# Optimization experiments

Measured on AMD Instinct MI355X. Metric: run time of the kernel, lower is better.

## Reference

```python
import jax, jax.numpy as jnp
import numpy as np

N = 50_000          # nodes (spots)
E = 800_000         # edges (~kNN degree 16)
IN_DIM, HID, OUT = 512, 64, 32
LEAKY = 0.2


def setup_inputs() -> dict:
    key = jax.random.key(0)
    ks = jax.random.split(key, 8)
    features = jax.random.normal(ks[0], (N, IN_DIM), dtype=jnp.float32)
    edge_index = jax.random.randint(ks[1], (2, E), 0, N, dtype=jnp.int64)
    # tied-weight GAT autoencoder parameters (xavier-normal, gain=1.414 as in stGCL)
    W1 = (jax.random.normal(ks[2], (IN_DIM, HID), dtype=jnp.float32)
          * np.float32(1.414 / np.sqrt(IN_DIM)))
    a1_src = jax.random.normal(ks[3], (HID,), dtype=jnp.float32) * 0.1
    a1_dst = jax.random.normal(ks[4], (HID,), dtype=jnp.float32) * 0.1
    W2 = (jax.random.normal(ks[5], (HID, OUT), dtype=jnp.float32)
          * np.float32(1.414 / np.sqrt(HID)))
    a3_src = jax.random.normal(ks[6], (HID,), dtype=jnp.float32) * 0.1
    a3_dst = jax.random.normal(ks[7], (HID,), dtype=jnp.float32) * 0.1
    return {"features": features, "edge_index": edge_index,
            "W1": W1, "a1_src": a1_src, "a1_dst": a1_dst,
            "W2": W2, "a3_src": a3_src, "a3_dst": a3_dst}


def reference(features, edge_index, W1, a1_src, a1_dst, W2, a3_src, a3_dst):
    src, dst = edge_index[0], edge_index[1]
    n = features.shape[0]

    # torch.randperm(features.size(0)) -> fixed-seed permutation
    perm = jax.random.permutation(jax.random.key(42), n)
    rand_features = features[perm]

    def gat(x, W, a_s, a_d):
        # stGCL GATConv (heads=1, concat=False, no self loops, no bias):
        # x_src = x_dst = x @ W; edge score = leaky_relu(a_s.xw[src] + a_d.xw[dst])
        xw = x @ W                                             # [N, C]
        e = jax.nn.leaky_relu((xw @ a_s)[src] + (xw @ a_d)[dst],
                              negative_slope=LEAKY)            # [E]
        # per-destination segment softmax (PyG softmax semantics)
        m = jax.ops.segment_max(e, dst, num_segments=n)        # [N]
        ex = jnp.exp(e - m[dst])
        denom = jax.ops.segment_sum(ex, dst, num_segments=n)
        alpha = ex / (denom[dst] + 1e-16)                      # [E]
        # weighted scatter-add aggregation
        return jax.ops.segment_sum(xw[src] * alpha[:, None], dst,
                                   num_segments=n)             # [N, C]

    def encode_decode(x):
        h1 = jax.nn.elu(gat(x, W1, a1_src, a1_dst))            # conv1, attention
        h2 = h1 @ W2                                           # conv2, attention=False
        h3 = jax.nn.elu(gat(h2, W2.T, a3_src, a3_dst))         # conv3 (tied W2^T), attention
        h4 = h3 @ W1.T                                         # conv4 (tied W1^T), attention=False
        return h2, h4

    h2, h4 = encode_decode(features)
    rand_h2, rand_h4 = encode_decode(rand_features)
    summary = jax.nn.sigmoid(h2.mean(axis=0))                  # [OUT]
    return (h2, h4, h4, rand_h2, rand_h4, rand_h4, summary)
```

## Files before the change

### kernel.cpp

```cpp
#include <hip/hip_runtime.h>
#include <hip/hip_bf16.h>
#include <vector>
#include <algorithm>
#include <cstring>
#include <cstdint>

#define NN 50000
#define EE 800000

static inline uint32_t rotl32(uint32_t v, int r) { return (v << r) | (v >> (32 - r)); }

static inline void tf2x32(uint32_t k0, uint32_t k1, uint32_t& x0, uint32_t& x1) {
  uint32_t ks0 = k0, ks1 = k1, ks2 = k0 ^ k1 ^ 0x1BD11BDAu;
  const int r1[4] = {13, 15, 26, 6}, r2[4] = {17, 29, 16, 24};
  x0 += ks0; x1 += ks1;
  for (int i = 0; i < 4; i++) { x0 += x1; x1 = rotl32(x1, r1[i]); x1 ^= x0; }
  x0 += ks1; x1 += ks2 + 1u;
  for (int i = 0; i < 4; i++) { x0 += x1; x1 = rotl32(x1, r2[i]); x1 ^= x0; }
  x0 += ks2; x1 += ks0 + 2u;
  for (int i = 0; i < 4; i++) { x0 += x1; x1 = rotl32(x1, r1[i]); x1 ^= x0; }
  x0 += ks0; x1 += ks1 + 3u;
  for (int i = 0; i < 4; i++) { x0 += x1; x1 = rotl32(x1, r2[i]); x1 ^= x0; }
  x0 += ks1; x1 += ks2 + 4u;
  for (int i = 0; i < 4; i++) { x0 += x1; x1 = rotl32(x1, r1[i]); x1 ^= x0; }
  x0 += ks2; x1 += ks0 + 5u;
}

static void compute_perm(int* perm, int n) {
  std::vector<uint32_t> sk(n);
  std::vector<int> val(n), order(n), nv(n);
  for (int i = 0; i < n; i++) val[i] = i;
  uint32_t k0 = 0u, k1 = 42u;
  for (int round = 0; round < 2; ++round) {
    uint32_t nk0, nk1, sk0, sk1;
    { uint32_t a = 0, b = 0; tf2x32(k0, k1, a, b); nk0 = a; nk1 = b; }
    { uint32_t a = 0, b = 1; tf2x32(k0, k1, a, b); sk0 = a; sk1 = b; }
    for (int i = 0; i < n; i++) {
      uint32_t a = 0, b = (uint32_t)i;
      tf2x32(sk0, sk1, a, b);
      sk[i] = a ^ b;
    }
    for (int i = 0; i < n; i++) order[i] = i;
    std::stable_sort(order.begin(), order.end(),
                     [&](int x, int y) { return sk[x] < sk[y]; });
    for (int i = 0; i < n; i++) nv[i] = val[order[i]];
    val.swap(nv);
    k0 = nk0; k1 = nk1;
  }
  std::memcpy(perm, val.data(), (size_t)n * sizeof(int));
}

struct PermHolder {
  int perm[NN];
  PermHolder() { compute_perm(perm, NN); }
};
static const PermHolder g_perm;


__global__ void count_kernel(const int* __restrict__ ei, int* __restrict__ counts, int E) {
  int e = blockIdx.x * 256 + threadIdx.x;
  if (e < E) atomicAdd(&counts[ei[E + e]], 1);
}

__global__ __launch_bounds__(1024) void scan_kernel(const int* __restrict__ counts,
                                                    int* __restrict__ offsets, int n) {
  __shared__ int wsum[16];
  __shared__ int wscan[16];
  __shared__ int carry_s;
  int tid = threadIdx.x, lane = tid & 63, wid = tid >> 6;
  if (tid == 0) carry_s = 0;
  __syncthreads();
  for (int base = 0; base < n; base += 1024) {
    int i = base + tid;
    int v = (i < n) ? counts[i] : 0;
    int x = v;
    #pragma unroll
    for (int off = 1; off < 64; off <<= 1) {
      int t = __shfl_up(x, off);
      if (lane >= off) x += t;
    }
    if (lane == 63) wsum[wid] = x;
    __syncthreads();
    if (wid == 0) {
      int wv = (lane < 16) ? wsum[lane] : 0;
      #pragma unroll
      for (int off = 1; off < 16; off <<= 1) {
        int t = __shfl_up(wv, off);
        if (lane >= off) wv += t;
      }
      if (lane < 16) wscan[lane] = wv;
    }
    __syncthreads();
    int wbase = (wid == 0) ? 0 : wscan[wid - 1];
    int carry = carry_s;
    if (i < n) offsets[i] = carry + wbase + x - v;
    int total = wscan[15];
    __syncthreads();
    if (tid == 0) carry_s = carry + total;
    __syncthreads();
  }
  if (threadIdx.x == 0) offsets[n] = carry_s;
}

__global__ void scatter_kernel(const int* __restrict__ ei, const int* __restrict__ offsets,
                               int* __restrict__ cursor, int* __restrict__ srcs, int E) {
  int e = blockIdx.x * 256 + threadIdx.x;
  if (e >= E) return;
  int s = ei[e];
  int d = ei[E + e];
  int pos = offsets[d] + atomicAdd(&cursor[d], 1);
  srcs[pos] = s;
}

__global__ __launch_bounds__(256) void gemm1_kernel(const float* __restrict__ A,
                                                    const float* __restrict__ B,
                                                    float* __restrict__ C,
                                                    const int* __restrict__ gather, int n) {
  __shared__ float As[32][68];
  __shared__ float Bs[32][68];
  int t = threadIdx.x;
  int m0 = blockIdx.x * 64;
  int tr = t >> 4, tc = t & 15;
  float acc[4][4] = {};
  for (int k0 = 0; k0 < 512; k0 += 32) {
    #pragma unroll
    for (int q = 0; q < 2; ++q) {
      int f = t + q * 256;
      int r = f >> 3, kq = f & 7;
      int row = m0 + r; row = (row < n) ? row : (n - 1);
      int g = gather ? gather[row] : row;
      const float4 av = *(const float4*)(A + (size_t)g * 512 + k0 + kq * 4);
      As[kq * 4 + 0][r] = av.x; As[kq * 4 + 1][r] = av.y;
      As[kq * 4 + 2][r] = av.z; As[kq * 4 + 3][r] = av.w;
    }
    #pragma unroll
    for (int q = 0; q < 2; ++q) {
      int f = t + q * 256;
      int kk = f >> 4, cq = f & 15;
      const float4 bv = *(const float4*)(B + (size_t)(k0 + kk) * 64 + cq * 4);
      *(float4*)(&Bs[kk][cq * 4]) = bv;
    }
    __syncthreads();
    #pragma unroll
    for (int kk = 0; kk < 32; ++kk) {
      float a[4], b[4];
      #pragma unroll
      for (int i = 0; i < 4; i++) a[i] = As[kk][tr * 4 + i];
      #pragma unroll
      for (int j = 0; j < 4; j++) b[j] = Bs[kk][tc * 4 + j];
      #pragma unroll
      for (int i = 0; i < 4; i++)
        #pragma unroll
        for (int j = 0; j < 4; j++) acc[i][j] += a[i] * b[j];
    }
    __syncthreads();
  }
  #pragma unroll
  for (int i = 0; i < 4; i++) {
    int row = m0 + tr * 4 + i;
    if (row < n) {
      float4 v = {acc[i][0], acc[i][1], acc[i][2], acc[i][3]};
      *(float4*)(C + (size_t)row * 64 + tc * 4) = v;
    }
  }
}

__global__ void dots_kernel(const float* __restrict__ xw, const float* __restrict__ a_src,
                            const float* __restrict__ a_dst, float* __restrict__ s,
                            float* __restrict__ d, int n) {
  int w = (blockIdx.x * blockDim.x + threadIdx.x) >> 6;
  int lane = threadIdx.x & 63;
  if (w >= n) return;
  float v = xw[(size_t)w * 64 + lane];
  float vs = v * a_src[lane], vd = v * a_dst[lane];
  #pragma unroll
  for (int off = 32; off; off >>= 1) {
    vs += __shfl_down(vs, off);
    vd += __shfl_down(vd, off);
  }
  if (lane == 0) { s[w] = vs; d[w] = vd; }
}

__global__ __launch_bounds__(256) void gat_kernel(const int* __restrict__ offs,
                                                  const int* __restrict__ srcs,
                                                  const float* __restrict__ s,
                                                  const float* __restrict__ dvec,
                                                  const float* __restrict__ xw,
                                                  float* __restrict__ h, int n) {
  int w = (blockIdx.x * blockDim.x + threadIdx.x) >> 6;
  int lane = threadIdx.x & 63;
  if (w >= n) return;
  int start = offs[w], end = offs[w + 1];
  float dd = dvec[w];
  float m = -INFINITY;
  for (int j = start + lane; j < end; j += 64) {
    float e = s[srcs[j]] + dd;
    e = e > 0.f ? e : 0.2f * e;
    m = fmaxf(m, e);
  }
  #pragma unroll
  for (int off = 32; off; off >>= 1) m = fmaxf(m, __shfl_xor(m, off));
  float sum = 0.f;
  for (int j = start + lane; j < end; j += 64) {
    float e = s[srcs[j]] + dd;
    e = e > 0.f ? e : 0.2f * e;
    sum += __expf(e - m);
  }
  #pragma unroll
  for (int off = 32; off; off >>= 1) sum += __shfl_xor(sum, off);
  float inv = 1.0f / (sum + 1e-16f);
  float acc = 0.f;
  for (int j = start; j < end; ++j) {
    int sj = srcs[j];
    float e = s[sj] + dd;
    e = e > 0.f ? e : 0.2f * e;
    float alpha = __expf(e - m) * inv;
    acc += alpha * xw[(size_t)sj * 64 + lane];
  }
  h[(size_t)w * 64 + lane] = acc > 0.f ? acc : expm1f(acc);
}

__global__ void gemm2_kernel(const float* __restrict__ h1, const float* __restrict__ W2,
                             float* __restrict__ h2, int n) {
  int id = blockIdx.x * 256 + threadIdx.x;
  if (id >= n * 32) return;
  int i = id >> 5, c = id & 31;
  float sacc = 0.f;
  #pragma unroll
  for (int k = 0; k < 64; k++) sacc += h1[(size_t)i * 64 + k] * W2[k * 32 + c];
  h2[id] = sacc;
}

__global__ void gemm3_kernel(const float* __restrict__ h2, const float* __restrict__ W2,
                             float* __restrict__ xw3, int n) {
  int id = blockIdx.x * 256 + threadIdx.x;
  if (id >= n * 64) return;
  int i = id >> 6, c = id & 63;
  float sacc = 0.f;
  #pragma unroll
  for (int j = 0; j < 32; j++) sacc += h2[(size_t)i * 32 + j] * W2[c * 32 + j];
  xw3[id] = sacc;
}

__global__ __launch_bounds__(256) void gemm4_kernel(const float* __restrict__ A,
                                                    const float* __restrict__ W1,
                                                    float* __restrict__ C0,
                                                    float* __restrict__ C1, int n) {
  __shared__ float As[64][68];
  __shared__ float Bs[64][68];
  int t = threadIdx.x;
  int m0 = blockIdx.x * 64;
  int o0 = blockIdx.y * 64;
  int tr = t >> 4, tc = t & 15;
  #pragma unroll
  for (int q = 0; q < 4; ++q) {
    int f = t + q * 256;
    int r = f >> 4, cq = f & 15;
    int row = m0 + r; row = (row < n) ? row : (n - 1);
    const float4 av = *(const float4*)(A + (size_t)row * 64 + cq * 4);
    As[cq * 4 + 0][r] = av.x; As[cq * 4 + 1][r] = av.y;
    As[cq * 4 + 2][r] = av.z; As[cq * 4 + 3][r] = av.w;
  }
  #pragma unroll
  for (int q = 0; q < 4; ++q) {
    int f = t + q * 256;
    int o = f >> 4, cq = f & 15;
    const float4 wv = *(const float4*)(W1 + (size_t)(o0 + o) * 64 + cq * 4);
    Bs[cq * 4 + 0][o] = wv.x; Bs[cq * 4 + 1][o] = wv.y;
    Bs[cq * 4 + 2][o] = wv.z; Bs[cq * 4 + 3][o] = wv.w;
  }
  __syncthreads();
  float acc[4][4] = {};
  #pragma unroll
  for (int kk = 0; kk < 64; ++kk) {
    float a[4], b[4];
    #pragma unroll
    for (int i = 0; i < 4; i++) a[i] = As[kk][tr * 4 + i];
    #pragma unroll
    for (int j = 0; j < 4; j++) b[j] = Bs[kk][tc * 4 + j];
    #pragma unroll
    for (int i = 0; i < 4; i++)
      #pragma unroll
      for (int j = 0; j < 4; j++) acc[i][j] += a[i] * b[j];
  }
  #pragma unroll
  for (int i = 0; i < 4; i++) {
    int row = m0 + tr * 4 + i;
    if (row < n) {
      float4 v = {acc[i][0], acc[i][1], acc[i][2], acc[i][3]};
      *(float4*)(C0 + (size_t)row * 512 + o0 + tc * 4) = v;
      *(float4*)(C1 + (size_t)row * 512 + o0 + tc * 4) = v;
    }
  }
}

__global__ void colsum_kernel(const float* __restrict__ h2, float* __restrict__ acc, int n) {
  int c = threadIdx.x & 31;
  int rg = (blockIdx.x << 3) + (threadIdx.x >> 5);
  float sloc = 0.f;
  for (int r = rg; r < n; r += 2048) sloc += h2[(size_t)r * 32 + c];
  atomicAdd(&acc[c], sloc);
}

__global__ void finalize_kernel(const float* __restrict__ acc, float* __restrict__ outp, int n) {
  int c = threadIdx.x;
  if (c < 32) {
    float mval = acc[c] / (float)n;
    outp[c] = 1.0f / (1.0f + __expf(-mval));
  }
}

extern "C" void kernel_launch(void* const* d_in, const int* in_sizes, int n_in,
                              void* d_out, int out_size, void* d_ws, size_t ws_size,
                              hipStream_t stream) {
  const float* features = (const float*)d_in[0];
  const int*   ei       = (const int*)d_in[1];
  const float* W1       = (const float*)d_in[2];
  const float* a1s      = (const float*)d_in[3];
  const float* a1d      = (const float*)d_in[4];
  const float* W2       = (const float*)d_in[5];
  const float* a3s      = (const float*)d_in[6];
  const float* a3d      = (const float*)d_in[7];
  float* out = (float*)d_out;

  const size_t NOUT = (size_t)NN * 32;
  const size_t NH4  = (size_t)NN * 512;
  const size_t OFF1 = NOUT;
  const size_t OFF2 = OFF1 + NH4;
  const size_t OFF3 = OFF2 + NH4;
  const size_t OFF4 = OFF3 + NOUT;
  const size_t OFF5 = OFF4 + NH4;
  const size_t OFF6 = OFF5 + NH4;

  char* w = (char*)d_ws;
  size_t o = 0;
  auto alloc = [&](size_t bytes) -> void* {
    void* p = w + o;
    o = (o + bytes + 255) & ~(size_t)255;
    return p;
  };
  int*   d_perm  = (int*)alloc((size_t)NN * 4);
  int*   counts  = (int*)alloc((size_t)NN * 4);
  int*   offsets = (int*)alloc((size_t)(NN + 1) * 4);
  int*   cursor  = (int*)alloc((size_t)NN * 4);
  int*   srcs    = (int*)alloc((size_t)EE * 4);
  float* xw      = (float*)alloc((size_t)NN * 64 * 4);
  float* hbuf    = (float*)alloc((size_t)NN * 64 * 4);
  float* sbuf    = (float*)alloc((size_t)NN * 4);
  float* dbuf    = (float*)alloc((size_t)NN * 4);
  float* accbuf  = (float*)alloc(32 * 4);

  hipMemcpyAsync(d_perm, g_perm.perm, (size_t)NN * 4, hipMemcpyHostToDevice, stream);
  hipMemsetAsync(counts, 0, (size_t)NN * 4, stream);
  hipMemsetAsync(cursor, 0, (size_t)NN * 4, stream);
  hipMemsetAsync(accbuf, 0, 32 * 4, stream);

  count_kernel<<<(EE + 255) / 256, 256, 0, stream>>>(ei, counts, EE);
  scan_kernel<<<1, 1024, 0, stream>>>(counts, offsets, NN);
  scatter_kernel<<<(EE + 255) / 256, 256, 0, stream>>>(ei, offsets, cursor, srcs, EE);

  const int rowBlocks = (NN + 63) / 64;
  const int nodeWaveBlocks = (NN * 64 + 255) / 256;

  for (int b = 0; b < 2; ++b) {
    const int* g = b ? d_perm : nullptr;
    float* h2out = out + (b ? OFF3 : 0);
    float* h4a   = out + (b ? OFF4 : OFF1);
    float* h4b   = out + (b ? OFF5 : OFF2);

    gemm1_kernel<<<rowBlocks, 256, 0, stream>>>(features, W1, xw, g, NN);
    dots_kernel<<<nodeWaveBlocks, 256, 0, stream>>>(xw, a1s, a1d, sbuf, dbuf, NN);
    gat_kernel<<<nodeWaveBlocks, 256, 0, stream>>>(offsets, srcs, sbuf, dbuf, xw, hbuf, NN);
    gemm2_kernel<<<(NN * 32 + 255) / 256, 256, 0, stream>>>(hbuf, W2, h2out, NN);
    gemm3_kernel<<<(NN * 64 + 255) / 256, 256, 0, stream>>>(h2out, W2, xw, NN);
    dots_kernel<<<nodeWaveBlocks, 256, 0, stream>>>(xw, a3s, a3d, sbuf, dbuf, NN);
    gat_kernel<<<nodeWaveBlocks, 256, 0, stream>>>(offsets, srcs, sbuf, dbuf, xw, hbuf, NN);
    gemm4_kernel<<<dim3(rowBlocks, 8), 256, 0, stream>>>(hbuf, W1, h4a, h4b, NN);
  }

  colsum_kernel<<<256, 256, 0, stream>>>(out, accbuf, NN);
  finalize_kernel<<<1, 64, 0, stream>>>(accbuf, out + OFF6, NN);
}
```

Baseline: 1.602 ms.

## Replace global-atomic CSR build with chunked LDS histogram counting sort

Replaces the global atomic count and scatter that build the destination-sorted edge list with a two-pass chunked counting sort. Per-chunk histograms are kept in LDS as packed 16-bit pairs, reduced and prefix-summed into per-chunk base offsets, and then each chunk scatters sources using LDS atomics for their ranks. This aims to remove contention on global atomics and to make the edge order within each destination deterministic. In exchange it adds kernels and a large per-chunk base array (CHUNKS*NN words) that must be written and read, and the 16-bit packing limits per-chunk degree.

```diff
diff --git a/kernel.cpp b/kernel.cpp
--- a/kernel.cpp
+++ b/kernel.cpp
@@ -7,6 +7,12 @@
 
 #define NN 50000
 #define EE 800000
+
+#define CHUNKS 128
+#define CHUNK_E (EE / CHUNKS)
+#define PAIRS (NN / 2)
+#define HALF (NN / 2)
+#define HPAIRS (HALF / 2)
 
 static inline uint32_t rotl32(uint32_t v, int r) { return (v << r) | (v >> (32 - r)); }
 
@@ -57,9 +63,35 @@
 static const PermHolder g_perm;
 
 
-__global__ void count_kernel(const int* __restrict__ ei, int* __restrict__ counts, int E) {
-  int e = blockIdx.x * 256 + threadIdx.x;
-  if (e < E) atomicAdd(&counts[ei[E + e]], 1);
+__global__ __launch_bounds__(256) void hist_kernel(const int* __restrict__ ei,
+                                                   uint32_t* __restrict__ hist) {
+  __shared__ uint32_t cnt[HPAIRS];
+  int b = blockIdx.x, c = b >> 1, h = b & 1;
+  for (int i = threadIdx.x; i < HPAIRS; i += 256) cnt[i] = 0;
+  __syncthreads();
+  int e0 = c * CHUNK_E;
+  int dlo = h * HALF;
+  for (int t = threadIdx.x; t < CHUNK_E; t += 256) {
+    int d = ei[EE + e0 + t];
+    int dl = d - dlo;
+    if ((unsigned)dl < (unsigned)HALF)
+      atomicAdd(&cnt[dl >> 1], (dl & 1) ? 0x10000u : 1u);
+  }
+  __syncthreads();
+  uint32_t* outp = hist + (size_t)c * PAIRS + (size_t)h * HPAIRS;
+  for (int i = threadIdx.x; i < HPAIRS; i += 256) outp[i] = cnt[i];
+}
+
+__global__ void counts_kernel(const uint32_t* __restrict__ hist, int* __restrict__ counts) {
+  int dp = blockIdx.x * 256 + threadIdx.x;
+  if (dp >= PAIRS) return;
+  uint32_t lo = 0, hi = 0;
+  for (int c = 0; c < CHUNKS; ++c) {
+    uint32_t p = hist[(size_t)c * PAIRS + dp];
+    lo += p & 0xFFFFu; hi += p >> 16;
+  }
+  counts[2 * dp] = (int)lo;
+  counts[2 * dp + 1] = (int)hi;
 }
 
 __global__ __launch_bounds__(1024) void scan_kernel(const int* __restrict__ counts,
@@ -102,14 +134,40 @@
   if (threadIdx.x == 0) offsets[n] = carry_s;
 }
 
-__global__ void scatter_kernel(const int* __restrict__ ei, const int* __restrict__ offsets,
-                               int* __restrict__ cursor, int* __restrict__ srcs, int E) {
-  int e = blockIdx.x * 256 + threadIdx.x;
-  if (e >= E) return;
-  int s = ei[e];
-  int d = ei[E + e];
-  int pos = offsets[d] + atomicAdd(&cursor[d], 1);
-  srcs[pos] = s;
+__global__ void base_kernel(const uint32_t* __restrict__ hist, const int* __restrict__ offsets,
+                            uint32_t* __restrict__ basearr) {
+  int dp = blockIdx.x * 256 + threadIdx.x;
+  if (dp >= PAIRS) return;
+  uint32_t r0 = (uint32_t)offsets[2 * dp];
+  uint32_t r1 = (uint32_t)offsets[2 * dp + 1];
+  for (int c = 0; c < CHUNKS; ++c) {
+    uint32_t p = hist[(size_t)c * PAIRS + dp];
+    basearr[(size_t)c * NN + 2 * dp] = r0;
+    basearr[(size_t)c * NN + 2 * dp + 1] = r1;
+    r0 += p & 0xFFFFu; r1 += p >> 16;
+  }
+}
+
+__global__ __launch_bounds__(256) void scatter2_kernel(const int* __restrict__ ei,
+                                                       const uint32_t* __restrict__ basearr,
+                                                       int* __restrict__ srcs) {
+  __shared__ uint32_t cnt[HPAIRS];
+  int b = blockIdx.x, c = b >> 1, h = b & 1;
+  for (int i = threadIdx.x; i < HPAIRS; i += 256) cnt[i] = 0;
+  __syncthreads();
+  int e0 = c * CHUNK_E;
+  int dlo = h * HALF;
+  const uint32_t* baserow = basearr + (size_t)c * NN;
+  for (int t = threadIdx.x; t < CHUNK_E; t += 256) {
+    int s = ei[e0 + t];
+    int d = ei[EE + e0 + t];
+    int dl = d - dlo;
+    if ((unsigned)dl < (unsigned)HALF) {
+      uint32_t old = atomicAdd(&cnt[dl >> 1], (dl & 1) ? 0x10000u : 1u);
+      uint32_t rank = (dl & 1) ? (old >> 16) : (old & 0xFFFFu);
+      srcs[baserow[d] + rank] = s;
+    }
+  }
 }
 
 __global__ __launch_bounds__(256) void gemm1_kernel(const float* __restrict__ A,
@@ -339,25 +397,26 @@
     o = (o + bytes + 255) & ~(size_t)255;
     return p;
   };
-  int*   d_perm  = (int*)alloc((size_t)NN * 4);
-  int*   counts  = (int*)alloc((size_t)NN * 4);
-  int*   offsets = (int*)alloc((size_t)(NN + 1) * 4);
-  int*   cursor  = (int*)alloc((size_t)NN * 4);
-  int*   srcs    = (int*)alloc((size_t)EE * 4);
-  float* xw      = (float*)alloc((size_t)NN * 64 * 4);
-  float* hbuf    = (float*)alloc((size_t)NN * 64 * 4);
-  float* sbuf    = (float*)alloc((size_t)NN * 4);
-  float* dbuf    = (float*)alloc((size_t)NN * 4);
-  float* accbuf  = (float*)alloc(32 * 4);
+  int*      d_perm  = (int*)alloc((size_t)NN * 4);
+  int*      counts  = (int*)alloc((size_t)NN * 4);
+  int*      offsets = (int*)alloc((size_t)(NN + 1) * 4);
+  int*      srcs    = (int*)alloc((size_t)EE * 4);
+  uint32_t* hist    = (uint32_t*)alloc((size_t)CHUNKS * PAIRS * 4);
+  uint32_t* basearr = (uint32_t*)alloc((size_t)CHUNKS * NN * 4);
+  float*    xw      = (float*)alloc((size_t)NN * 64 * 4);
+  float*    hbuf    = (float*)alloc((size_t)NN * 64 * 4);
+  float*    sbuf    = (float*)alloc((size_t)NN * 4);
+  float*    dbuf    = (float*)alloc((size_t)NN * 4);
+  float*    accbuf  = (float*)alloc(32 * 4);
 
   hipMemcpyAsync(d_perm, g_perm.perm, (size_t)NN * 4, hipMemcpyHostToDevice, stream);
-  hipMemsetAsync(counts, 0, (size_t)NN * 4, stream);
-  hipMemsetAsync(cursor, 0, (size_t)NN * 4, stream);
   hipMemsetAsync(accbuf, 0, 32 * 4, stream);
 
-  count_kernel<<<(EE + 255) / 256, 256, 0, stream>>>(ei, counts, EE);
+  hist_kernel<<<CHUNKS * 2, 256, 0, stream>>>(ei, hist);
+  counts_kernel<<<(PAIRS + 255) / 256, 256, 0, stream>>>(hist, counts);
   scan_kernel<<<1, 1024, 0, stream>>>(counts, offsets, NN);
-  scatter_kernel<<<(EE + 255) / 256, 256, 0, stream>>>(ei, offsets, cursor, srcs, EE);
+  base_kernel<<<(PAIRS + 255) / 256, 256, 0, stream>>>(hist, offsets, basearr);
+  scatter2_kernel<<<CHUNKS * 2, 256, 0, stream>>>(ei, basearr, srcs);
 
   const int rowBlocks = (NN + 63) / 64;
   const int nodeWaveBlocks = (NN * 64 + 255) / 256;
```

Result: no change. 1.596 ms (-0.4%).
